# Performance work log

Hardware: AMD Instinct MI355X
Metric: run time of the kernel (lower is better)

Reference implementation:

```python
import jax, jax.numpy as jnp
import numpy as np

T = 36  # num_frames


def box_cxcywh_to_xyxy(b):
    cx, cy, w, h = jnp.split(b, 4, axis=-1)
    return jnp.concatenate([cx - 0.5 * w, cy - 0.5 * h, cx + 0.5 * w, cy + 0.5 * h], axis=-1)


def multi_iou(b1, b2):
    # b1: [Q,1,T,4], b2: [1,N,T,4], xyxy -> iou [Q,N,T]
    lt = jnp.maximum(b1[..., :2], b2[..., :2])
    rb = jnp.minimum(b1[..., 2:], b2[..., 2:])
    wh = jnp.clip(rb - lt, 0.0)
    inter = wh[..., 0] * wh[..., 1]
    a1 = (b1[..., 2] - b1[..., 0]) * (b1[..., 3] - b1[..., 1])
    a2 = (b2[..., 2] - b2[..., 0]) * (b2[..., 3] - b2[..., 1])
    union = a1 + a2 - inter
    return inter / union


def setup_inputs() -> dict:
    key = jax.random.key(0)
    k1, k2, k3, k4, k5, k6 = jax.random.split(key, 6)
    Q, N, C = 2048, 128, 42
    return {
        "pred_logits": jax.random.normal(k1, (T * Q, C), dtype=jnp.float32),
        "pred_boxes": jax.random.uniform(k2, (T * Q, 4), dtype=jnp.float32),
        "tgt_labels": jax.random.randint(k3, (N * T,), 0, C - 1),
        "tgt_boxes": jax.random.uniform(k4, (N * T, 4), dtype=jnp.float32),
        "tgt_valid": jax.random.randint(k5, (N * T,), 0, 2, dtype=jnp.int32),
        "tgt_original_valid": jax.random.randint(k6, (N * T,), 0, 2, dtype=jnp.int32),
    }


def reference(pred_logits, pred_boxes, tgt_labels, tgt_boxes, tgt_valid, tgt_original_valid):
    # Cost-matrix computation of SoftMaxHungarianMatcher (cost_class=cost_bbox=cost_giou=1,
    # use_giou=False, use_l1_distance_sum=False). The scipy linear_sum_assignment step is
    # CPU-serial / non-tensor and excluded; output is the [Q,N] cost fed to it.
    C = pred_logits.shape[-1]
    Q = pred_logits.shape[0] // T
    N = tgt_labels.shape[0] // T
    num_classes = C - 1  # background index

    probs = jax.nn.softmax(pred_logits, axis=-1).reshape(T, Q, C).transpose(1, 0, 2)  # [Q,T,C]
    boxes = pred_boxes.reshape(T, Q, 4).transpose(1, 0, 2)                            # [Q,T,4]
    tboxes = tgt_boxes.reshape(N, T, 4)
    valid = tgt_valid.reshape(N, T).astype(probs.dtype)                               # [N,T]
    ovalid = tgt_original_valid.reshape(N, T)
    ids = jnp.where(ovalid == 0, num_classes, tgt_labels.reshape(N, T))               # [N,T]

    denom = valid.sum(-1)  # [N] (per-instance count of valid frames)

    # class cost: -mean_t p(q, t, ids[n,t]) over valid frames
    gathered = probs[:, jnp.arange(T)[None, :], ids]                                  # [Q,N,T]
    class_cost = -(gathered * valid).sum(-1) / denom                                  # [Q,N]

    # bbox L1 cost: mean over (valid frames, 4 coords)
    l1 = jnp.abs(boxes[:, None] - tboxes[None]).mean(-1)                              # [Q,N,T]
    bbox_cost = (l1 * valid).sum(-1) / denom                                          # [Q,N]

    # IoU cost: -mean_t iou over valid frames
    iou = multi_iou(box_cxcywh_to_xyxy(boxes)[:, None], box_cxcywh_to_xyxy(tboxes)[None])
    iou_cost = -(iou * valid).sum(-1) / denom                                         # [Q,N]

    return class_cost + bbox_cost + iou_cost
```

## Files before the change

kernel.cpp:

```cpp
#include <hip/hip_runtime.h>
#include <hip/hip_bf16.h>


constexpr int T = 36;
constexpr int Q = 2048;
constexpr int C = 42;
constexpr int N = 128;

__global__ __launch_bounds__(256) void softmax_transpose_kernel(
    const float* __restrict__ logits, __hip_bfloat16* __restrict__ P2) {
  constexpr int QB = 64;
  constexpr int LS = C + 1;

  __shared__ float tile[QB * LS];
  __shared__ float s_max[4 * QB];
  __shared__ float s_sum[4 * QB];
  __shared__ float s_rinv[QB];

  const int t = blockIdx.y;
  const int q0 = blockIdx.x * QB;
  const int tid = threadIdx.x;

  const float* src = logits + ((size_t)t * Q + q0) * C;
  for (int i = tid; i < QB * C; i += 256) {
    int r = i / C, c = i % C;
    tile[r * LS + c] = src[i];
  }
  __syncthreads();

  const int part = tid >> 6;
  const int row = tid & 63;
  const int c0 = (part < 2) ? part * 11 : 22 + (part - 2) * 10;
  const int c1 = (part < 2) ? c0 + 11 : c0 + 10;

  float m = -1e30f;
  for (int c = c0; c < c1; ++c) m = fmaxf(m, tile[row * LS + c]);
  s_max[part * QB + row] = m;
  __syncthreads();

  m = fmaxf(fmaxf(s_max[row], s_max[QB + row]),
            fmaxf(s_max[2 * QB + row], s_max[3 * QB + row]));
  float s = 0.f;
  for (int c = c0; c < c1; ++c) {
    float e = __expf(tile[row * LS + c] - m);
    tile[row * LS + c] = e;
    s += e;
  }
  s_sum[part * QB + row] = s;
  __syncthreads();

  if (part == 0) {
    float stot = s_sum[row] + s_sum[QB + row] + s_sum[2 * QB + row] +
                 s_sum[3 * QB + row];
    s_rinv[row] = 1.f / stot;
  }
  __syncthreads();

  for (int i = tid; i < QB * C / 2; i += 256) {
    int c = i >> 5;
    int r2 = i & 31;
    float v0 = tile[(2 * r2) * LS + c] * s_rinv[2 * r2];
    float v1 = tile[(2 * r2 + 1) * LS + c] * s_rinv[2 * r2 + 1];
    __hip_bfloat162 pk;
    pk.x = __float2bfloat16(v0);
    pk.y = __float2bfloat16(v1);
    *(__hip_bfloat162*)(P2 + (size_t)(t * C + c) * Q + q0 + 2 * r2) = pk;
  }
}

constexpr int NB = 8;

__global__ __launch_bounds__(512) void cost_kernel(
    const __hip_bfloat16* __restrict__ P2, const float* __restrict__ pred_boxes,
    const int* __restrict__ labels, const float* __restrict__ tboxes,
    const int* __restrict__ valid, const int* __restrict__ ovalid,
    float* __restrict__ out) {
  constexpr int RS = NB + 1;

  const int q0 = blockIdx.x * 64;
  const int n0 = blockIdx.y * NB;
  const int tid = threadIdx.x;
  const int lane = tid & 63;
  const int wave = tid >> 6;
  const int q = q0 + lane;

  __shared__ float4 s_tbA[NB * T];
  __shared__ float4 s_tbB[NB * T];
  __shared__ int s_pk[NB * T];
  __shared__ float s_rden[NB];
  __shared__ float s_red[8 * 64 * RS];

  for (int i = tid; i < NB * T; i += 512) {
    int n = n0 + i / T;
    int t = i % T;
    int g = n * T + t;
    int id = (ovalid[g] == 0) ? (C - 1) : labels[g];
    s_pk[i] = (valid[g] << 24) | (id * (Q * 2));
    float4 tb = ((const float4*)tboxes)[g];
    s_tbA[i] = tb;
    float4 B;
    B.x = fmaf(-0.5f, tb.z, tb.x);
    B.y = fmaf(-0.5f, tb.w, tb.y);
    B.z = fmaf(0.5f, tb.z, tb.x);
    B.w = fmaf(0.5f, tb.w, tb.y);
    s_tbB[i] = B;
  }
  if (tid < NB) {
    int n = n0 + tid;
    int s = 0;
    for (int t = 0; t < T; ++t) s += valid[n * T + t];
    s_rden[tid] = 1.f / (float)s;
  }
  __syncthreads();

  float acc[NB];
#pragma unroll
  for (int j = 0; j < NB; ++j) acc[j] = 0.f;

  const int t_begin = (wave * T) / 8;
  const int t_end = ((wave + 1) * T) / 8;

  for (int t = t_begin; t < t_end; ++t) {
    float4 pb = ((const float4*)pred_boxes)[t * Q + q];
    float px1 = fmaf(-0.5f, pb.z, pb.x);
    float py1 = fmaf(-0.5f, pb.w, pb.y);
    float px2 = fmaf(0.5f, pb.z, pb.x);
    float py2 = fmaf(0.5f, pb.w, pb.y);
    float area_p = pb.z * pb.w;
    const char* pcol = (const char*)(P2 + (size_t)t * C * Q + q);

#pragma unroll
    for (int j = 0; j < NB; ++j) {
      int pk = s_pk[j * T + t];
      if (pk & (1 << 24)) {
        float4 tb = s_tbA[j * T + t];
        float4 xy = s_tbB[j * T + t];
        float p = __bfloat162float(
            *(const __hip_bfloat16*)(pcol + (pk & 0xFFFFFF)));

        float s = fabsf(pb.x - tb.x) + fabsf(pb.y - tb.y) +
                  fabsf(pb.z - tb.z) + fabsf(pb.w - tb.w);
        float iw = fmaxf(fminf(px2, xy.z) - fmaxf(px1, xy.x), 0.f);
        float ih = fmaxf(fminf(py2, xy.w) - fmaxf(py1, xy.y), 0.f);
        float inter = iw * ih;
        float uni = fmaf(tb.z, tb.w, area_p) - inter;
        float r = __builtin_amdgcn_rcpf(uni);
        acc[j] = fmaf(0.25f, s, acc[j]) - p - inter * r;
      }
    }
  }

#pragma unroll
  for (int j = 0; j < NB; ++j) s_red[(wave * 64 + lane) * RS + j] = acc[j];
  __syncthreads();

  {
    int ql = tid >> 3;
    int j = tid & 7;
    float s = 0.f;
#pragma unroll
    for (int w = 0; w < 8; ++w) s += s_red[(w * 64 + ql) * RS + j];
    out[(size_t)(q0 + ql) * N + n0 + j] = s * s_rden[j];
  }
}

extern "C" void kernel_launch(void* const* d_in, const int* in_sizes, int n_in,
                              void* d_out, int out_size, void* d_ws, size_t ws_size,
                              hipStream_t stream) {
  const float* logits = (const float*)d_in[0];
  const float* pboxes = (const float*)d_in[1];
  const int* labels = (const int*)d_in[2];
  const float* tboxes = (const float*)d_in[3];
  const int* valid = (const int*)d_in[4];
  const int* ovalid = (const int*)d_in[5];
  float* out = (float*)d_out;

  __hip_bfloat16* P2 = (__hip_bfloat16*)d_ws;

  dim3 g1(Q / 64, T);
  softmax_transpose_kernel<<<g1, 256, 0, stream>>>(logits, P2);

  dim3 g2(Q / 64, N / NB);
  cost_kernel<<<g2, 512, 0, stream>>>(P2, pboxes, labels, tboxes, valid, ovalid, out);
}
```

Baseline: 86.27 us.

## Process two query columns per thread and make cost loop branchless

Each cost_kernel thread now handles two queries (q and q+64), so every shared-memory read of target box data is reused twice and the grid is halved. The per-target valid-frame branch becomes a multiply by the valid flag. The L1 term is recomputed from xyxy differences, which drops the separate cxcywh target copy. The reduction stage now writes float2 pairs. The cost is more registers for the doubled accumulators, fewer blocks for occupancy, and extra arithmetic on invalid frames.

```diff
diff --git a/kernel.cpp b/kernel.cpp
--- a/kernel.cpp
+++ b/kernel.cpp
@@ -77,33 +77,33 @@
     float* __restrict__ out) {
   constexpr int RS = NB + 1;
 
-  const int q0 = blockIdx.x * 64;
+  const int q0 = blockIdx.x * 128;
   const int n0 = blockIdx.y * NB;
   const int tid = threadIdx.x;
   const int lane = tid & 63;
   const int wave = tid >> 6;
-  const int q = q0 + lane;
-
-  __shared__ float4 s_tbA[NB * T];
-  __shared__ float4 s_tbB[NB * T];
-  __shared__ int s_pk[NB * T];
+  const int qA = q0 + lane;
+
+  __shared__ float4 s_xy[NB * T];
+  __shared__ float2 s_av[NB * T];
+  __shared__ int s_off[NB * T];
   __shared__ float s_rden[NB];
-  __shared__ float s_red[8 * 64 * RS];
+  __shared__ float s_red[8 * 128 * RS];
 
   for (int i = tid; i < NB * T; i += 512) {
     int n = n0 + i / T;
     int t = i % T;
     int g = n * T + t;
     int id = (ovalid[g] == 0) ? (C - 1) : labels[g];
-    s_pk[i] = (valid[g] << 24) | (id * (Q * 2));
+    s_off[i] = id * (Q * 2);
     float4 tb = ((const float4*)tboxes)[g];
-    s_tbA[i] = tb;
     float4 B;
     B.x = fmaf(-0.5f, tb.z, tb.x);
     B.y = fmaf(-0.5f, tb.w, tb.y);
     B.z = fmaf(0.5f, tb.z, tb.x);
     B.w = fmaf(0.5f, tb.w, tb.y);
-    s_tbB[i] = B;
+    s_xy[i] = B;
+    s_av[i] = make_float2(tb.z * tb.w, (float)valid[g]);
   }
   if (tid < NB) {
     int n = n0 + tid;
@@ -113,54 +113,86 @@
   }
   __syncthreads();
 
-  float acc[NB];
-#pragma unroll
-  for (int j = 0; j < NB; ++j) acc[j] = 0.f;
+  float accA[NB], accB[NB];
+#pragma unroll
+  for (int j = 0; j < NB; ++j) accA[j] = accB[j] = 0.f;
 
   const int t_begin = (wave * T) / 8;
   const int t_end = ((wave + 1) * T) / 8;
 
   for (int t = t_begin; t < t_end; ++t) {
-    float4 pb = ((const float4*)pred_boxes)[t * Q + q];
-    float px1 = fmaf(-0.5f, pb.z, pb.x);
-    float py1 = fmaf(-0.5f, pb.w, pb.y);
-    float px2 = fmaf(0.5f, pb.z, pb.x);
-    float py2 = fmaf(0.5f, pb.w, pb.y);
-    float area_p = pb.z * pb.w;
-    const char* pcol = (const char*)(P2 + (size_t)t * C * Q + q);
-
+    float4 pa = ((const float4*)pred_boxes)[t * Q + qA];
+    float4 pb = ((const float4*)pred_boxes)[t * Q + qA + 64];
+    float ax1 = fmaf(-0.5f, pa.z, pa.x), ay1 = fmaf(-0.5f, pa.w, pa.y);
+    float ax2 = fmaf(0.5f, pa.z, pa.x), ay2 = fmaf(0.5f, pa.w, pa.y);
+    float aarea = pa.z * pa.w;
+    float bx1 = fmaf(-0.5f, pb.z, pb.x), by1 = fmaf(-0.5f, pb.w, pb.y);
+    float bx2 = fmaf(0.5f, pb.z, pb.x), by2 = fmaf(0.5f, pb.w, pb.y);
+    float barea = pb.z * pb.w;
+
+    const char* pcol = (const char*)(P2 + (size_t)t * C * Q + qA);
+
+    float pA[NB], pB[NB];
 #pragma unroll
     for (int j = 0; j < NB; ++j) {
-      int pk = s_pk[j * T + t];
-      if (pk & (1 << 24)) {
-        float4 tb = s_tbA[j * T + t];
-        float4 xy = s_tbB[j * T + t];
-        float p = __bfloat162float(
-            *(const __hip_bfloat16*)(pcol + (pk & 0xFFFFFF)));
-
-        float s = fabsf(pb.x - tb.x) + fabsf(pb.y - tb.y) +
-                  fabsf(pb.z - tb.z) + fabsf(pb.w - tb.w);
-        float iw = fmaxf(fminf(px2, xy.z) - fmaxf(px1, xy.x), 0.f);
-        float ih = fmaxf(fminf(py2, xy.w) - fmaxf(py1, xy.y), 0.f);
+      int off = s_off[j * T + t];
+      pA[j] = __bfloat162float(*(const __hip_bfloat16*)(pcol + off));
+      pB[j] = __bfloat162float(*(const __hip_bfloat16*)(pcol + off + 128));
+    }
+
+#pragma unroll
+    for (int j = 0; j < NB; ++j) {
+      float4 xy = s_xy[j * T + t];
+      float2 av = s_av[j * T + t];
+      {
+        float d1 = ax1 - xy.x, d2 = ax2 - xy.z;
+        float d3 = ay1 - xy.y, d4 = ay2 - xy.w;
+        float sL = fabsf(d1 + d2) + fabsf(d3 + d4);
+        float sW = fabsf(d2 - d1) + fabsf(d4 - d3);
+        float iw = fmaxf(fminf(ax2, xy.z) - fmaxf(ax1, xy.x), 0.f);
+        float ih = fmaxf(fminf(ay2, xy.w) - fmaxf(ay1, xy.y), 0.f);
         float inter = iw * ih;
-        float uni = fmaf(tb.z, tb.w, area_p) - inter;
-        float r = __builtin_amdgcn_rcpf(uni);
-        acc[j] = fmaf(0.25f, s, acc[j]) - p - inter * r;
+        float uni = (aarea + av.x) - inter;
+        float iou = inter * __builtin_amdgcn_rcpf(uni);
+        float term = fmaf(0.125f, sL, fmaf(0.25f, sW, -pA[j])) - iou;
+        accA[j] = fmaf(av.y, term, accA[j]);
+      }
+      {
+        float d1 = bx1 - xy.x, d2 = bx2 - xy.z;
+        float d3 = by1 - xy.y, d4 = by2 - xy.w;
+        float sL = fabsf(d1 + d2) + fabsf(d3 + d4);
+        float sW = fabsf(d2 - d1) + fabsf(d4 - d3);
+        float iw = fmaxf(fminf(bx2, xy.z) - fmaxf(bx1, xy.x), 0.f);
+        float ih = fmaxf(fminf(by2, xy.w) - fmaxf(by1, xy.y), 0.f);
+        float inter = iw * ih;
+        float uni = (barea + av.x) - inter;
+        float iou = inter * __builtin_amdgcn_rcpf(uni);
+        float term = fmaf(0.125f, sL, fmaf(0.25f, sW, -pB[j]));
+        accB[j] = fmaf(av.y, term - iou, accB[j]);
       }
     }
   }
 
 #pragma unroll
-  for (int j = 0; j < NB; ++j) s_red[(wave * 64 + lane) * RS + j] = acc[j];
+  for (int j = 0; j < NB; ++j) {
+    s_red[(wave * 128 + lane) * RS + j] = accA[j];
+    s_red[(wave * 128 + 64 + lane) * RS + j] = accB[j];
+  }
   __syncthreads();
 
   {
-    int ql = tid >> 3;
-    int j = tid & 7;
-    float s = 0.f;
-#pragma unroll
-    for (int w = 0; w < 8; ++w) s += s_red[(w * 64 + ql) * RS + j];
-    out[(size_t)(q0 + ql) * N + n0 + j] = s * s_rden[j];
+    int oq = tid >> 2;
+    int jp = (tid & 3) * 2;
+    float s0 = 0.f, s1 = 0.f;
+#pragma unroll
+    for (int w = 0; w < 8; ++w) {
+      s0 += s_red[(w * 128 + oq) * RS + jp];
+      s1 += s_red[(w * 128 + oq) * RS + jp + 1];
+    }
+    float2 o;
+    o.x = s0 * s_rden[jp];
+    o.y = s1 * s_rden[jp + 1];
+    *(float2*)(out + (size_t)(q0 + oq) * N + n0 + jp) = o;
   }
 }
 
@@ -180,6 +212,6 @@
   dim3 g1(Q / 64, T);
   softmax_transpose_kernel<<<g1, 256, 0, stream>>>(logits, P2);
 
-  dim3 g2(Q / 64, N / NB);
+  dim3 g2(Q / 128, N / NB);
   cost_kernel<<<g2, 512, 0, stream>>>(P2, pboxes, labels, tboxes, valid, ovalid, out);
 }
```

Result: slower. 88.24 us (+2.3%).
